# Optimization experiments

Hardware: AMD Instinct MI355X
Metric: run time of the kernel (lower is better)

The kernel has to match this reference:

```python
import jax, jax.numpy as jnp
import numpy as np
from jax import lax

WS = 32          # region_size
N = WS * WS      # tokens per region = 1024
H = 8            # num_heads
HD = 64          # head_dim
C = H * HD       # dim = 512
B = 8            # num_regions * batch
K = 15           # conv_k
SCALE = HD ** -0.5


def _rel_index():
    # Swin relative position index, computed statically with numpy.
    coords = np.stack(np.meshgrid(np.arange(WS), np.arange(WS), indexing='ij'))  # [2,WS,WS]
    flat = coords.reshape(2, -1)                                                 # [2,N]
    rel = (flat[:, :, None] - flat[:, None, :]).transpose(1, 2, 0)               # [N,N,2]
    rel = rel.copy()
    rel[..., 0] += WS - 1
    rel[..., 1] += WS - 1
    rel[..., 0] *= 2 * WS - 1
    return rel.sum(-1)  # [N,N] int

_REL_IDX = jnp.asarray(_rel_index())


def setup_inputs() -> dict:
    key = jax.random.key(0)
    ks = jax.random.split(key, 6)
    return {
        'x': jax.random.normal(ks[0], (B, N, C), dtype=jnp.float32),
        'w_qkv': jax.random.normal(ks[1], (3 * C, C), dtype=jnp.float32) * 0.02,
        'b_qkv': jnp.zeros((3 * C,), dtype=jnp.float32),
        'w_proj': jax.random.normal(ks[2], (C, C), dtype=jnp.float32) * 0.02,
        'b_proj': jnp.zeros((C,), dtype=jnp.float32),
        'rel_table': jax.random.normal(ks[3], ((2 * WS - 1) ** 2, H), dtype=jnp.float32) * 0.02,
        'pe_w': jax.random.normal(ks[4], (H, 1, K, 1), dtype=jnp.float32) * 0.02,
        'pe_b': jnp.zeros((H,), dtype=jnp.float32),
    }


def reference(x, w_qkv, b_qkv, w_proj, b_proj, rel_table, pe_w, pe_b):
    b, n, c = x.shape
    qkv = (x @ w_qkv.T + b_qkv).reshape(b, n, 3, H, HD)
    q = jnp.moveaxis(qkv[:, :, 0], 2, 1)  # [B,H,N,HD]
    k = jnp.moveaxis(qkv[:, :, 1], 2, 1)
    v = jnp.moveaxis(qkv[:, :, 2], 2, 1)

    attn = jnp.einsum('bhnd,bhmd->bhnm', q * SCALE, k)  # [B,H,N,N]

    # depthwise (per-head) conv over the query axis of the attention matrix, kernel (K,1)
    pe = lax.conv_general_dilated(
        attn, pe_w, window_strides=(1, 1), padding=[(K // 2, K // 2), (0, 0)],
        dimension_numbers=('NCHW', 'OIHW', 'NCHW'), feature_group_count=H,
    ) + pe_b[None, :, None, None]
    attn = attn + pe

    # relative position bias gather: [N*N] -> [N,N,H] -> [H,N,N]
    bias = rel_table[_REL_IDX.reshape(-1)].reshape(n, n, H).transpose(2, 0, 1)
    attn = jax.nn.softmax(attn + bias[None], axis=-1)

    out = jnp.einsum('bhnm,bhmd->bnhd', attn, v).reshape(b, n, c)
    return out @ w_proj.T + b_proj
```

## Files before the change

### kernel.cpp

```cpp
#include <hip/hip_runtime.h>

typedef __bf16 bf16x8 __attribute__((ext_vector_type(8)));
typedef float f32x4 __attribute__((ext_vector_type(4)));
typedef unsigned short u16;
typedef unsigned int u32;
typedef unsigned long long u64;

__device__ __forceinline__ float bf2f(u16 x){ u32 u = ((u32)x)<<16; return __builtin_bit_cast(float,u); }
__device__ __forceinline__ u16 f2bf(float f){ u32 u = __builtin_bit_cast(u32,f); u = (u + 0x7fffu + ((u>>16)&1u)) >> 16; return (u16)u; }

__device__ __forceinline__ void glds16(const u16* g, u16* l){
  __builtin_amdgcn_global_load_lds((const __attribute__((address_space(1))) u32*)g,
                                   (__attribute__((address_space(3))) u32*)l, 16, 0, 0);
}

static constexpr float L2E = 1.4426950408889634f;
static constexpr float QSC = 0.125f * 1.4426950408889634f;

__global__ void k_cvtall(const float* __restrict__ x, const float* __restrict__ wq,
                         const float* __restrict__ wp, const float* __restrict__ rt,
                         u16* __restrict__ xo, u16* __restrict__ wqo,
                         u16* __restrict__ wpo, u16* __restrict__ relo){
  int bid = blockIdx.x;
  if (bid < 5120){
    int i = bid*256 + threadIdx.x;
    const float* s; u16* d; int base;
    if (i < 1048576){ s=x; d=xo; base=0; }
    else if (i < 1245184){ s=wq; d=wqo; base=1048576; }
    else { s=wp; d=wpo; base=1245184; }
    int j = i - base;
    float4 v = reinterpret_cast<const float4*>(s)[j];
    reinterpret_cast<ushort4*>(d)[j] = make_ushort4(f2bf(v.x),f2bf(v.y),f2bf(v.z),f2bf(v.w));
  } else {
    int i = (bid-5120)*256 + threadIdx.x;
    if (i < 31752){
      int h = i / 3969, i2 = i - h*3969;
      relo[i] = f2bf(rt[i2*8+h]*L2E);
    }
  }
}

__device__ __forceinline__ void acc8(float* acc, uint4 v, float w){
  acc[0]=fmaf(w, bf2f((u16)(v.x)),     acc[0]); acc[1]=fmaf(w, bf2f((u16)(v.x>>16)), acc[1]);
  acc[2]=fmaf(w, bf2f((u16)(v.y)),     acc[2]); acc[3]=fmaf(w, bf2f((u16)(v.y>>16)), acc[3]);
  acc[4]=fmaf(w, bf2f((u16)(v.z)),     acc[4]); acc[5]=fmaf(w, bf2f((u16)(v.z>>16)), acc[5]);
  acc[6]=fmaf(w, bf2f((u16)(v.w)),     acc[6]); acc[7]=fmaf(w, bf2f((u16)(v.w>>16)), acc[7]);
}
__global__ void k_qconv(const u16* __restrict__ q, u16* __restrict__ qp, const float* __restrict__ pw){
  int idx = blockIdx.x*256 + threadIdx.x;
  int dc = idx&7, n = (idx>>3)&1023, bh = idx>>13, h = bh&7;
  const u16* base = q + (long)bh*65536 + dc*8;
  float wgt[15];
  #pragma unroll
  for (int t=0;t<15;t++) wgt[t] = pw[h*15+t];
  float acc[8];
  {
    uint4 cv = *reinterpret_cast<const uint4*>(base + n*64);
    acc[0]=bf2f((u16)cv.x); acc[1]=bf2f((u16)(cv.x>>16));
    acc[2]=bf2f((u16)cv.y); acc[3]=bf2f((u16)(cv.y>>16));
    acc[4]=bf2f((u16)cv.z); acc[5]=bf2f((u16)(cv.z>>16));
    acc[6]=bf2f((u16)cv.w); acc[7]=bf2f((u16)(cv.w>>16));
  }
  #pragma unroll
  for (int t=0;t<15;t++){
    int nn = n - 7 + t;
    if (nn >= 0 && nn < 1024){
      uint4 v = *reinterpret_cast<const uint4*>(base + nn*64);
      acc8(acc, v, wgt[t]);
    }
  }
  u16* out = qp + (long)bh*65536 + n*64 + dc*8;
  *reinterpret_cast<ushort4*>(out)   = make_ushort4(f2bf(acc[0]),f2bf(acc[1]),f2bf(acc[2]),f2bf(acc[3]));
  *reinterpret_cast<ushort4*>(out+4) = make_ushort4(f2bf(acc[4]),f2bf(acc[5]),f2bf(acc[6]),f2bf(acc[7]));
}

template<int MODE>
__global__ __launch_bounds__(256) void k_gemm(
  const u16* __restrict__ A, const u16* __restrict__ Bw, const float* __restrict__ bias,
  u16* __restrict__ qo, u16* __restrict__ ko, u16* __restrict__ vo, float* __restrict__ co)
{
  constexpr int K = 512;
  constexpr int NX = (MODE==0) ? 12 : 4;
  constexpr int CPX = NX*64/8;
  __shared__ __align__(16) u16 lA[3][4096];
  __shared__ __align__(16) u16 lB[3][4096];
  const int lin = blockIdx.y*NX + blockIdx.x;
  const int swz = (lin&7)*CPX + (lin>>3);
  const int i0 = (swz/NX)*128, j0 = (swz%NX)*128;
  const int T = threadIdx.x;
  const int w = T>>6, lane = T&63, g = lane>>4, cl = lane&15;
  const int wr = (w>>1)*64, wc = (w&1)*64;
  const int sr = T>>2, sk = 8*(T&3);
  f32x4 acc[4][4];
  #pragma unroll
  for (int a=0;a<4;a++)
    #pragma unroll
    for (int b=0;b<4;b++) acc[a][b] = (f32x4){0.f,0.f,0.f,0.f};

  auto STAGE = [&](int t, u16* bA, u16* bB){
    glds16(A  + (long)(i0+sr)*K    + t*32 + sk, bA + 8*T);
    glds16(A  + (long)(i0+64+sr)*K + t*32 + sk, bA + 2048 + 8*T);
    glds16(Bw + (long)(j0+sr)*K    + t*32 + sk, bB + 8*T);
    glds16(Bw + (long)(j0+64+sr)*K + t*32 + sk, bB + 2048 + 8*T);
  };
  STAGE(0, lA[0], lB[0]);
  STAGE(1, lA[1], lB[1]);
  int cur = 0, sb = 2;
  for (int t=0;t<16;t++){
    if (t<14){
      STAGE(t+2, lA[sb], lB[sb]);
      asm volatile("s_waitcnt vmcnt(8)" ::: "memory");
    } else if (t==14){
      asm volatile("s_waitcnt vmcnt(4)" ::: "memory");
    } else {
      asm volatile("s_waitcnt vmcnt(0)" ::: "memory");
    }
    __builtin_amdgcn_s_barrier();
    const u16* cA = lA[cur];
    const u16* cB = lB[cur];
    bf16x8 af[4], bfr[4];
    #pragma unroll
    for (int mf=0;mf<4;mf++) af[mf]  = *reinterpret_cast<const bf16x8*>(cA + (wr+16*mf+cl)*32 + 8*g);
    #pragma unroll
    for (int nf=0;nf<4;nf++) bfr[nf] = *reinterpret_cast<const bf16x8*>(cB + (wc+16*nf+cl)*32 + 8*g);
    __builtin_amdgcn_s_setprio(1);
    #pragma unroll
    for (int mf=0;mf<4;mf++)
      #pragma unroll
      for (int nf=0;nf<4;nf++)
        acc[mf][nf] = __builtin_amdgcn_mfma_f32_16x16x32_bf16(af[mf], bfr[nf], acc[mf][nf], 0,0,0);
    __builtin_amdgcn_s_setprio(0);
    __builtin_amdgcn_s_barrier();
    asm volatile("" ::: "memory");
    cur = (cur==2)?0:cur+1;
    sb  = (sb==2)?0:sb+1;
  }

  #pragma unroll
  for (int mf=0;mf<4;mf++){
    #pragma unroll
    for (int nf=0;nf<4;nf++){
      const int col = j0 + wc + 16*nf + cl;
      const float bb = bias[col];
      const int row0 = i0 + wr + 16*mf + 4*g;
      if (MODE==0){
        const int part = col>>9, h=(col>>6)&7, dd=col&63;
        const int b = row0>>10, n0 = row0&1023, bh = b*8+h;
        if (part==2){
          const int a32 = n0 & ~31, G = (n0>>2)&7;
          const int stb = ((G&3)<<3) | ((G>>2)<<2);
          ushort4 pk = make_ushort4(f2bf(acc[mf][nf][0]+bb), f2bf(acc[mf][nf][1]+bb),
                                    f2bf(acc[mf][nf][2]+bb), f2bf(acc[mf][nf][3]+bb));
          *reinterpret_cast<ushort4*>(vo + ((long)bh*64+dd)*1024 + a32 + stb) = pk;
        } else {
          #pragma unroll
          for (int e=0;e<4;e++){
            float v = acc[mf][nf][e] + bb;
            if (part==0) qo[((long)bh*1024+n0+e)*64+dd] = f2bf(v*QSC);
            else         ko[((long)bh*1024+n0+e)*64+dd] = f2bf(v);
          }
        }
      } else {
        #pragma unroll
        for (int e=0;e<4;e++)
          co[(long)(row0+e)*512 + col] = acc[mf][nf][e] + bb;
      }
    }
  }
}

__global__ __launch_bounds__(256,2) void k_attn(
  const u16* __restrict__ Qp, const u16* __restrict__ Kb, const u16* __restrict__ VT,
  const u16* __restrict__ relT, u16* __restrict__ Ao)
{
  __shared__ __align__(16) u16 kls[3][4096];
  __shared__ __align__(16) u16 vls[3][4096];
  const int bid = blockIdx.x;
  const int xcd = bid&7, slot = bid>>3;
  const int bh = xcd*8 + (slot>>3), rb = slot&7;
  const int b = bh>>3, h = bh&7;
  const int T = threadIdx.x, w=T>>6, lane=T&63, g=lane>>4, cl=lane&15;
  const int rowbase = rb*128 + w*32;
  const int qr[2] = { rowbase + cl, rowbase + 16 + cl };
  bf16x8 qf[2][2];
  #pragma unroll
  for (int G=0;G<2;G++){
    const u16* Qr = Qp + ((long)bh*1024 + qr[G])*64;
    qf[G][0] = *reinterpret_cast<const bf16x8*>(Qr + 8*g);
    qf[G][1] = *reinterpret_cast<const bf16x8*>(Qr + 32 + 8*g);
  }
  const int rt[2] = { (qr[0]>>5)*63 + (qr[0]&31) + 1984,
                      (qr[1]>>5)*63 + (qr[1]&31) + 1984 };
  const u16* relTh = relT + h*3969;
  const u16* Kbh = Kb + (long)bh*65536;
  const u16* Vbh = VT + (long)bh*65536;
  float lsum[2] = {0.f, 0.f};
  f32x4 oacc[2][4];
  #pragma unroll
  for (int G=0;G<2;G++)
    #pragma unroll
    for (int c=0;c<4;c++) oacc[G][c] = (f32x4){0.f,0.f,0.f,0.f};

  auto STAGE = [&](int m0, u16* kbuf, u16* vbuf){
    #pragma unroll
    for (int s=0;s<2;s++){
      int idx = s*256 + T, row = idx>>3, u = idx&7, sw = (u ^ (row&7))<<3;
      glds16(Kbh + (m0+row)*64 + sw,         kbuf + idx*8);
      glds16(Vbh + (long)row*1024 + m0 + sw, vbuf + idx*8);
    }
  };
  STAGE(0,  kls[0], vls[0]);
  STAGE(64, kls[1], vls[1]);

  int cur = 0, sb = 2;
  for (int t=0;t<16;t++){
    const int m0 = t<<6;
    u16 rv[2][4][4];
    #pragma unroll
    for (int G=0;G<2;G++)
      #pragma unroll
      for (int c=0;c<4;c++){
        const int kk = m0 + 16*c + 4*g;
        const int ridx = rt[G] - ((kk>>5)*63 + (kk&31));
        #pragma unroll
        for (int e=0;e<4;e++) rv[G][c][e] = relTh[ridx - e];
      }
    asm volatile("" ::: "memory");
    if (t<14){
      STAGE(m0+128, kls[sb], vls[sb]);
      asm volatile("s_waitcnt vmcnt(40)" ::: "memory");
    } else if (t==14){
      asm volatile("s_waitcnt vmcnt(36)" ::: "memory");
    } else {
      asm volatile("s_waitcnt vmcnt(32)" ::: "memory");
    }
    __builtin_amdgcn_s_barrier();

    const char* kb = (const char*)kls[cur];
    const char* vb = (const char*)vls[cur];
    f32x4 sacc[2][4];
    #pragma unroll
    for (int G=0;G<2;G++)
      #pragma unroll
      for (int c=0;c<4;c++) sacc[G][c] = (f32x4){0.f,0.f,0.f,0.f};
    __builtin_amdgcn_s_setprio(1);
    #pragma unroll
    for (int c=0;c<4;c++){
      const int r = 16*c + cl, rs = r&7;
      const char* kr = kb + r*128;
      bf16x8 kf0 = *reinterpret_cast<const bf16x8*>(kr + ((g    ^rs)<<4));
      bf16x8 kf1 = *reinterpret_cast<const bf16x8*>(kr + (((4+g)^rs)<<4));
      #pragma unroll
      for (int G=0;G<2;G++){
        sacc[G][c] = __builtin_amdgcn_mfma_f32_16x16x32_bf16(kf0, qf[G][0], sacc[G][c],0,0,0);
        sacc[G][c] = __builtin_amdgcn_mfma_f32_16x16x32_bf16(kf1, qf[G][1], sacc[G][c],0,0,0);
      }
    }
    __builtin_amdgcn_s_setprio(0);
    float p[2][4][4];
    #pragma unroll
    for (int G=0;G<2;G++)
      #pragma unroll
      for (int c=0;c<4;c++)
        #pragma unroll
        for (int e=0;e<4;e++){
          float bias = __builtin_bit_cast(float, ((u32)rv[G][c][e])<<16);
          p[G][c][e] = __builtin_amdgcn_exp2f(sacc[G][c][e] + bias);
        }
    #pragma unroll
    for (int G=0;G<2;G++)
      #pragma unroll
      for (int c=0;c<4;c++) lsum[G] += (p[G][c][0]+p[G][c][1]) + (p[G][c][2]+p[G][c][3]);
    bf16x8 pa[2][2];
    #pragma unroll
    for (int G=0;G<2;G++)
      #pragma unroll
      for (int e=0;e<4;e++){
        pa[G][0][e]   = (__bf16)p[G][0][e];  pa[G][0][4+e] = (__bf16)p[G][1][e];
        pa[G][1][e]   = (__bf16)p[G][2][e];  pa[G][1][4+e] = (__bf16)p[G][3][e];
      }
    __builtin_amdgcn_s_setprio(1);
    #pragma unroll
    for (int ks=0;ks<2;ks++)
      #pragma unroll
      for (int c2=0;c2<4;c2++){
        const int dd = 16*c2 + cl, dsw = dd&7;
        bf16x8 vf = *reinterpret_cast<const bf16x8*>(vb + dd*128 + (((4*ks+g)^dsw)<<4));
        #pragma unroll
        for (int G=0;G<2;G++)
          oacc[G][c2] = __builtin_amdgcn_mfma_f32_16x16x32_bf16(pa[G][ks], vf, oacc[G][c2],0,0,0);
      }
    __builtin_amdgcn_s_setprio(0);
    __builtin_amdgcn_s_barrier();
    asm volatile("" ::: "memory");
    cur = (cur==2)?0:cur+1;
    sb  = (sb==2)?0:sb+1;
  }
  #pragma unroll
  for (int G=0;G<2;G++){
    lsum[G] += __shfl_xor(lsum[G], 16, 64);
    lsum[G] += __shfl_xor(lsum[G], 32, 64);
  }
  #pragma unroll
  for (int G=0;G<2;G++)
    #pragma unroll
    for (int e=0;e<4;e++){
      float inv = 1.0f/__shfl(lsum[G], 4*g+e, 64);
      const long orow = (long)b*1024 + rowbase + 16*G + 4*g + e;
      #pragma unroll
      for (int c2=0;c2<4;c2++)
        Ao[orow*512 + h*64 + 16*c2 + cl] = f2bf(oacc[G][c2][e]*inv);
    }
}

extern "C" void kernel_launch(void* const* d_in, const int* in_sizes, int n_in,
                              void* d_out, int out_size, void* d_ws, size_t ws_size,
                              hipStream_t stream)
{
  const float* x         = (const float*)d_in[0];
  const float* w_qkv     = (const float*)d_in[1];
  const float* b_qkv     = (const float*)d_in[2];
  const float* w_proj    = (const float*)d_in[3];
  const float* b_proj    = (const float*)d_in[4];
  const float* rel_table = (const float*)d_in[5];
  const float* pe_w      = (const float*)d_in[6];
  (void)in_sizes; (void)n_in; (void)out_size; (void)ws_size;

  u16* ws    = (u16*)d_ws;
  u16* x_bf  = ws;
  u16* wq_bf = x_bf  + 4194304;
  u16* wp_bf = wq_bf + 786432;
  u16* q_bf  = wp_bf + 262144;
  u16* k_bf  = q_bf  + 4194304;
  u16* vt_bf = k_bf  + 4194304;
  u16* qp_bf = vt_bf + 4194304;
  u16* ao_bf = qp_bf + 4194304;
  u16* relT  = ao_bf + 4194304;

  k_cvtall<<<5245,256,0,stream>>>(x, w_qkv, w_proj, rel_table, x_bf, wq_bf, wp_bf, relT);
  k_gemm<0><<<dim3(12,64),256,0,stream>>>(x_bf, wq_bf, b_qkv, q_bf, k_bf, vt_bf, nullptr);
  k_qconv<<<2048,256,0,stream>>>(q_bf, qp_bf, pe_w);
  k_attn<<<512,256,0,stream>>>(qp_bf, k_bf, vt_bf, relT, ao_bf);
  k_gemm<1><<<dim3(4,64),256,0,stream>>>(ao_bf, wp_bf, b_proj, nullptr, nullptr, nullptr, (float*)d_out);
}
```

Measured before the change: 85.81 us.

## Pack relative-bias quads as u64 and single-barrier pipelines in GEMM and attention

Precomputes the relative-position bias table as 64-bit words holding four consecutive bf16 entries, so attention does one 8-byte gather per fragment instead of four 2-byte gathers. Attention moves to a 4-deep K/V LDS ring with prefetch issued after one barrier per iteration. The GEMM is restructured the same way, issuing its next-stage loads after the barrier and dropping the second barrier. This cuts scattered global loads and barrier stalls, but attention LDS grows to 64 KB per block, which could limit occupancy, and the packed bias table is four times larger.

```diff
diff --git a/kernel.cpp b/kernel.cpp
--- a/kernel.cpp
+++ b/kernel.cpp
@@ -20,7 +20,7 @@
 __global__ void k_cvtall(const float* __restrict__ x, const float* __restrict__ wq,
                          const float* __restrict__ wp, const float* __restrict__ rt,
                          u16* __restrict__ xo, u16* __restrict__ wqo,
-                         u16* __restrict__ wpo, u16* __restrict__ relo){
+                         u16* __restrict__ wpo, u64* __restrict__ rel2){
   int bid = blockIdx.x;
   if (bid < 5120){
     int i = bid*256 + threadIdx.x;
@@ -35,7 +35,15 @@
     int i = (bid-5120)*256 + threadIdx.x;
     if (i < 31752){
       int h = i / 3969, i2 = i - h*3969;
-      relo[i] = f2bf(rt[i2*8+h]*L2E);
+      u64 v = 0;
+      #pragma unroll
+      for (int j=0;j<4;j++){
+        int idx = i2-3+j;
+        u16 bb = 0;
+        if (idx >= 0) bb = f2bf(rt[idx*8+h]*L2E);
+        v |= (u64)bb << (16*j);
+      }
+      rel2[i] = v;
     }
   }
 }
@@ -107,15 +115,11 @@
   STAGE(1, lA[1], lB[1]);
   int cur = 0, sb = 2;
   for (int t=0;t<16;t++){
-    if (t<14){
-      STAGE(t+2, lA[sb], lB[sb]);
-      asm volatile("s_waitcnt vmcnt(8)" ::: "memory");
-    } else if (t==14){
-      asm volatile("s_waitcnt vmcnt(4)" ::: "memory");
-    } else {
-      asm volatile("s_waitcnt vmcnt(0)" ::: "memory");
-    }
+    if (t<15) asm volatile("s_waitcnt vmcnt(4)" ::: "memory");
+    else      asm volatile("s_waitcnt vmcnt(0)" ::: "memory");
     __builtin_amdgcn_s_barrier();
+    asm volatile("" ::: "memory");
+    if (t<14) STAGE(t+2, lA[sb], lB[sb]);
     const u16* cA = lA[cur];
     const u16* cB = lB[cur];
     bf16x8 af[4], bfr[4];
@@ -130,8 +134,6 @@
       for (int nf=0;nf<4;nf++)
         acc[mf][nf] = __builtin_amdgcn_mfma_f32_16x16x32_bf16(af[mf], bfr[nf], acc[mf][nf], 0,0,0);
     __builtin_amdgcn_s_setprio(0);
-    __builtin_amdgcn_s_barrier();
-    asm volatile("" ::: "memory");
     cur = (cur==2)?0:cur+1;
     sb  = (sb==2)?0:sb+1;
   }
@@ -171,10 +173,10 @@
 
 __global__ __launch_bounds__(256,2) void k_attn(
   const u16* __restrict__ Qp, const u16* __restrict__ Kb, const u16* __restrict__ VT,
-  const u16* __restrict__ relT, u16* __restrict__ Ao)
+  const u64* __restrict__ relT2, u16* __restrict__ Ao)
 {
-  __shared__ __align__(16) u16 kls[3][4096];
-  __shared__ __align__(16) u16 vls[3][4096];
+  __shared__ __align__(16) u16 kls[4][4096];
+  __shared__ __align__(16) u16 vls[4][4096];
   const int bid = blockIdx.x;
   const int xcd = bid&7, slot = bid>>3;
   const int bh = xcd*8 + (slot>>3), rb = slot&7;
@@ -191,7 +193,7 @@
   }
   const int rt[2] = { (qr[0]>>5)*63 + (qr[0]&31) + 1984,
                       (qr[1]>>5)*63 + (qr[1]&31) + 1984 };
-  const u16* relTh = relT + h*3969;
+  const u64* relTh = relT2 + h*3969;
   const u16* Kbh = Kb + (long)bh*65536;
   const u16* Vbh = VT + (long)bh*65536;
   float lsum[2] = {0.f, 0.f};
@@ -201,43 +203,35 @@
     #pragma unroll
     for (int c=0;c<4;c++) oacc[G][c] = (f32x4){0.f,0.f,0.f,0.f};
 
-  auto STAGE = [&](int m0, u16* kbuf, u16* vbuf){
+  auto STAGE = [&](int m0, int bi){
     #pragma unroll
     for (int s=0;s<2;s++){
       int idx = s*256 + T, row = idx>>3, u = idx&7, sw = (u ^ (row&7))<<3;
-      glds16(Kbh + (m0+row)*64 + sw,         kbuf + idx*8);
-      glds16(Vbh + (long)row*1024 + m0 + sw, vbuf + idx*8);
+      glds16(Kbh + (m0+row)*64 + sw,         kls[bi] + idx*8);
+      glds16(Vbh + (long)row*1024 + m0 + sw, vls[bi] + idx*8);
     }
   };
-  STAGE(0,  kls[0], vls[0]);
-  STAGE(64, kls[1], vls[1]);
-
-  int cur = 0, sb = 2;
+  STAGE(0,0); STAGE(64,1); STAGE(128,2);
+
   for (int t=0;t<16;t++){
     const int m0 = t<<6;
-    u16 rv[2][4][4];
+    u64 rx[2][4];
     #pragma unroll
     for (int G=0;G<2;G++)
       #pragma unroll
       for (int c=0;c<4;c++){
         const int kk = m0 + 16*c + 4*g;
-        const int ridx = rt[G] - ((kk>>5)*63 + (kk&31));
-        #pragma unroll
-        for (int e=0;e<4;e++) rv[G][c][e] = relTh[ridx - e];
-      }
+        rx[G][c] = relTh[rt[G] - ((kk>>5)*63 + (kk&31))];
+      }
+    if (t<=13)      asm volatile("s_waitcnt vmcnt(16)" ::: "memory");
+    else if (t==14) asm volatile("s_waitcnt vmcnt(12)" ::: "memory");
+    else            asm volatile("s_waitcnt vmcnt(8)"  ::: "memory");
+    __builtin_amdgcn_s_barrier();
     asm volatile("" ::: "memory");
-    if (t<14){
-      STAGE(m0+128, kls[sb], vls[sb]);
-      asm volatile("s_waitcnt vmcnt(40)" ::: "memory");
-    } else if (t==14){
-      asm volatile("s_waitcnt vmcnt(36)" ::: "memory");
-    } else {
-      asm volatile("s_waitcnt vmcnt(32)" ::: "memory");
-    }
-    __builtin_amdgcn_s_barrier();
-
-    const char* kb = (const char*)kls[cur];
-    const char* vb = (const char*)vls[cur];
+    if (t<13) STAGE(m0+192, (t+3)&3);
+
+    const char* kb = (const char*)kls[t&3];
+    const char* vb = (const char*)vls[t&3];
     f32x4 sacc[2][4];
     #pragma unroll
     for (int G=0;G<2;G++)
@@ -264,7 +258,7 @@
       for (int c=0;c<4;c++)
         #pragma unroll
         for (int e=0;e<4;e++){
-          float bias = __builtin_bit_cast(float, ((u32)rv[G][c][e])<<16);
+          float bias = __builtin_bit_cast(float, ((u32)((u16)(rx[G][c] >> (16*(3-e)))))<<16);
           p[G][c][e] = __builtin_amdgcn_exp2f(sacc[G][c][e] + bias);
         }
     #pragma unroll
@@ -291,10 +285,6 @@
           oacc[G][c2] = __builtin_amdgcn_mfma_f32_16x16x32_bf16(pa[G][ks], vf, oacc[G][c2],0,0,0);
       }
     __builtin_amdgcn_s_setprio(0);
-    __builtin_amdgcn_s_barrier();
-    asm volatile("" ::: "memory");
-    cur = (cur==2)?0:cur+1;
-    sb  = (sb==2)?0:sb+1;
   }
   #pragma unroll
   for (int G=0;G<2;G++){
@@ -335,11 +325,11 @@
   u16* vt_bf = k_bf  + 4194304;
   u16* qp_bf = vt_bf + 4194304;
   u16* ao_bf = qp_bf + 4194304;
-  u16* relT  = ao_bf + 4194304;
-
-  k_cvtall<<<5245,256,0,stream>>>(x, w_qkv, w_proj, rel_table, x_bf, wq_bf, wp_bf, relT);
+  u64* relT2 = (u64*)(ao_bf + 4194304);
+
+  k_cvtall<<<5245,256,0,stream>>>(x, w_qkv, w_proj, rel_table, x_bf, wq_bf, wp_bf, relT2);
   k_gemm<0><<<dim3(12,64),256,0,stream>>>(x_bf, wq_bf, b_qkv, q_bf, k_bf, vt_bf, nullptr);
   k_qconv<<<2048,256,0,stream>>>(q_bf, qp_bf, pe_w);
-  k_attn<<<512,256,0,stream>>>(qp_bf, k_bf, vt_bf, relT, ao_bf);
+  k_attn<<<512,256,0,stream>>>(qp_bf, k_bf, vt_bf, relT2, ao_bf);
   k_gemm<1><<<dim3(4,64),256,0,stream>>>(ao_bf, wp_bf, b_proj, nullptr, nullptr, nullptr, (float*)d_out);
 }
```

Measured after the change: 84.18 us. About the same (-1.9%).
